# Kernel tuning notes

Hardware: AMD Instinct MI355X
Metric: run time of the kernel (lower is better)

Reference implementation:

```python
import jax, jax.numpy as jnp
import numpy as np

N = 100000
E = 1600000
IN_DIM = 1024
H_DIM = 16
DIM2 = H_DIM * 8  # 128


def _xavier(key, shape):
    fan_in, fan_out = shape[-2], shape[-1]
    lim = (6.0 / (fan_in + fan_out)) ** 0.5
    return jax.random.uniform(key, shape, jnp.float32, -lim, lim)


def setup_inputs() -> dict:
    key = jax.random.key(0)
    ks = jax.random.split(key, 10)
    x = jax.random.normal(ks[0], (N, IN_DIM), jnp.float32)
    edge_index = jax.random.randint(ks[1], (2, E), 0, N)
    perm = jax.random.permutation(ks[2], N)
    W1 = _xavier(ks[3], (IN_DIM, DIM2)); b1 = jnp.zeros((DIM2,), jnp.float32)
    W2 = _xavier(ks[4], (DIM2, DIM2)); b2 = jnp.zeros((DIM2,), jnp.float32)
    W3 = _xavier(ks[5], (DIM2, H_DIM)); b3 = jnp.zeros((H_DIM,), jnp.float32)
    Wdo = _xavier(ks[6], (1, DIM2, DIM2)); bdo = jnp.zeros((1,), jnp.float32)
    Wdh = _xavier(ks[7], (1, H_DIM, H_DIM)); bdh = jnp.zeros((1,), jnp.float32)
    return dict(x=x, W1=W1, b1=b1, W2=W2, b2=b2, W3=W3, b3=b3,
                Wdo=Wdo, bdo=bdo, Wdh=Wdh, bdh=bdh,
                edge_index=edge_index, perm=perm)


def _graph_conv(x, W, b, src, dst, norm_src, norm_dst):
    # DGL GraphConv, norm='both': D_dst^{-1/2} A D_src^{-1/2} X W + b
    h = (x * norm_src[:, None]) @ W          # mult W first (in >= out)
    agg = jax.ops.segment_sum(h[src], dst, num_segments=N)
    return agg * norm_dst[:, None] + b


def _l2norm(x):
    n = jnp.sqrt(jnp.sum(x * x, axis=1, keepdims=True))
    return x / jnp.maximum(n, 1e-12)


def _bilinear(a, c, W, b):
    # nn.Bilinear(n_h, n_h, 1): out[n,k] = a[n] @ W[k] @ c[n] + b[k]
    return jnp.einsum('nd,kde,ne->nk', a, W, c) + b


def reference(x, W1, b1, W2, b2, W3, b3, Wdo, bdo, Wdh, bdh, edge_index, perm):
    src, dst = edge_index[0], edge_index[1]
    ones = jnp.ones((E,), jnp.float32)
    deg_out = jnp.maximum(jax.ops.segment_sum(ones, src, num_segments=N), 1.0)
    deg_in = jnp.maximum(jax.ops.segment_sum(ones, dst, num_segments=N), 1.0)
    ns, nd = deg_out ** -0.5, deg_in ** -0.5

    def encode(xin):
        o = _graph_conv(xin, W1, b1, src, dst, ns, nd)
        o = _graph_conv(o, W2, b2, src, dst, ns, nd) + o
        h = _graph_conv(o, W3, b3, src, dst, ns, nd)
        emb_o = jax.nn.relu(o)
        g_o = jax.nn.sigmoid(_l2norm(emb_o))
        emb_h = jax.nn.relu(h)
        g_h = jax.nn.sigmoid(_l2norm(emb_h))
        return h, emb_o, g_o, emb_h, g_h

    h, emb_o, g_o, emb_h, g_h = encode(x)
    h_a, emb_oa, g_oa, emb_ha, g_ha = encode(x[perm])

    def disc(c, h_pl, h_mi, W, b):
        return jnp.concatenate([_bilinear(h_pl, c, W, b), _bilinear(h_mi, c, W, b)], axis=1)

    ret_o = disc(g_o, emb_o, emb_oa, Wdo, bdo)
    ret_oa = disc(g_oa, emb_oa, emb_o, Wdo, bdo)
    ret_h = disc(g_h, emb_h, emb_ha, Wdh, bdh)
    ret_ha = disc(g_ha, emb_ha, emb_h, Wdh, bdh)
    return (h, ret_o, ret_h, ret_oa, ret_ha)
```

## Files before the change

kernel.cpp:

```cpp
#include <hip/hip_runtime.h>
#include <math.h>

#define NN 100000
#define EE 1600000
#define SCB 98

typedef __attribute__((ext_vector_type(8))) short bf16x8;
typedef __attribute__((ext_vector_type(4))) short bf16x4;
typedef __attribute__((ext_vector_type(4))) float f32x4;

__device__ __forceinline__ unsigned short f2bf(float x){
  union { float f; unsigned u; } v; v.f = x;
  unsigned r = v.u + 0x7FFFu + ((v.u >> 16) & 1u);
  return (unsigned short)(r >> 16);
}
__device__ __forceinline__ float bf2f(unsigned short h){
  union { unsigned u; float f; } v; v.u = ((unsigned)h) << 16; return v.f;
}
__device__ __forceinline__ float sigm(float x){ return 1.0f/(1.0f+__expf(-x)); }

__device__ __forceinline__ void barrier_lds_only(){
  asm volatile("s_waitcnt lgkmcnt(0)" ::: "memory");
  __builtin_amdgcn_s_barrier();
  __builtin_amdgcn_sched_barrier(0);
}

__global__ __launch_bounds__(256) void k_deg_wcvt(const int* __restrict__ src, const int* __restrict__ dst,
                      int* __restrict__ dout, int* __restrict__ din,
                      const float* __restrict__ W1, const float* __restrict__ W2,
                      const float* __restrict__ Wdo, const float* __restrict__ W3,
                      unsigned short* __restrict__ W1T, unsigned short* __restrict__ W2T,
                      unsigned short* __restrict__ WdoB, unsigned short* __restrict__ W3c){
  int b = blockIdx.x;
  if (b < EE/256){
    int e = b*256 + threadIdx.x;
    atomicAdd(&dout[src[e]],1); atomicAdd(&din[dst[e]],1);
  } else {
    int i = (b - EE/256)*256 + threadIdx.x;
    if (i < 131072){
      int c = i>>13, r = i&8191, col = r>>6, k = c*64 + (r&63);
      W1T[i] = f2bf(W1[(size_t)k*128 + col]);
    } else if (i < 147456){
      int j = i-131072;
      int c = j>>13, r = j&8191, col = r>>6, k = c*64 + (r&63);
      W2T[j] = f2bf(W2[(size_t)k*128 + col]);
    } else if (i < 163840){
      int j = i-147456;
      int c = j>>13, r = j&8191, col = r>>6, k = c*64 + (r&63);
      WdoB[j] = f2bf(Wdo[(size_t)col*128 + k]);
    } else if (i < 165888){
      int j = i-163840;
      int col = j>>7, k = j&127;
      W3c[j] = f2bf(W3[(size_t)k*16 + col]);
    }
  }
}

__global__ __launch_bounds__(1024) void k_scan1(const int* __restrict__ din, int* __restrict__ chunk,
                        int* __restrict__ bsum){
  __shared__ int wsum[16];
  int t = threadIdx.x, lane = t & 63, w = t >> 6;
  int i = blockIdx.x*1024 + t;
  int v = (i < NN) ? din[i] : 0;
  int x = v;
  #pragma unroll
  for (int off=1; off<64; off<<=1){
    int y = __shfl_up(x, off);
    if (lane>=off) x += y;
  }
  if (lane==63) wsum[w] = x;
  __syncthreads();
  int pre = 0;
  #pragma unroll
  for (int j=0;j<16;j++) if (j<w) pre += wsum[j];
  int incl = x + pre;
  if (i < NN) chunk[i] = incl;
  if (t == 1023) bsum[blockIdx.x] = incl;
}

__global__ __launch_bounds__(128) void k_scan2(const int* __restrict__ bsum, int* __restrict__ bpre,
                       int* __restrict__ row_ptr){
  __shared__ int w0tot;
  int t = threadIdx.x, lane = t & 63, w = t >> 6;
  int v = (t < SCB) ? bsum[t] : 0;
  int x = v;
  #pragma unroll
  for (int off=1; off<64; off<<=1){
    int y = __shfl_up(x, off);
    if (lane>=off) x += y;
  }
  if (w==0 && lane==63) w0tot = x;
  __syncthreads();
  int incl = x + (w ? w0tot : 0);
  if (t < SCB) bpre[t] = incl - v;
  if (t == 0) row_ptr[0] = 0;
}

__global__ __launch_bounds__(256) void k_scan3(const int* __restrict__ din, const int* __restrict__ chunk,
                       const int* __restrict__ bpre, const int* __restrict__ dout,
                       const int* __restrict__ perm,
                       int* __restrict__ row_ptr, int* __restrict__ cursor,
                       float* __restrict__ ns, float* __restrict__ nd, int* __restrict__ inv){
  int i = blockIdx.x*256 + threadIdx.x;
  if (i < NN){
    int d = din[i];
    int val = chunk[i] + bpre[i>>10];
    row_ptr[i+1] = val;
    cursor[i] = val - d;
    ns[i] = rsqrtf((float)max(dout[i],1));
    nd[i] = rsqrtf((float)max(d,1));
    inv[perm[i]] = i;
  }
}

__global__ __launch_bounds__(256) void k_fill(const int* __restrict__ src, const int* __restrict__ dst,
                       int* __restrict__ cursor, int* __restrict__ col){
  int e = blockIdx.x*256+threadIdx.x;
  if (e<EE){ int pos = atomicAdd(&cursor[dst[e]],1); col[pos] = src[e]; }
}

struct ARF { float4 a, b; };
struct ARU { bf16x8 a; };
__device__ __forceinline__ void aload(ARF& r, const float* p){
  r.a = *(const float4*)p; r.b = *(const float4*)(p+4);
}
__device__ __forceinline__ void aload(ARU& r, const unsigned short* p){
  r.a = *(const bf16x8*)p;
}
template<int IM>
__device__ __forceinline__ bf16x8 aconv(const ARF& r, float rs){
  float av[8] = {r.a.x,r.a.y,r.a.z,r.a.w,r.b.x,r.b.y,r.b.z,r.b.w};
  if constexpr (IM==1){
    #pragma unroll
    for (int i=0;i<8;i++) av[i] = sigm(fmaxf(av[i],0.0f)*rs);
  }
  bf16x8 o;
  #pragma unroll
  for (int i=0;i<8;i++) o[i] = (short)f2bf(av[i]);
  return o;
}
template<int IM>
__device__ __forceinline__ bf16x8 aconv(const ARU& r, float rs){
  if constexpr (IM==0) return r.a;
  else {
    bf16x8 o;
    #pragma unroll
    for (int i=0;i<8;i++){
      float v = sigm(fmaxf(bf2f((unsigned short)r.a[i]),0.0f)*rs);
      o[i] = (short)f2bf(v);
    }
    return o;
  }
}
__device__ __forceinline__ bf16x8 araw(const ARU& r){ return r.a; }
__device__ __forceinline__ bf16x8 araw(const ARF& r){
  bf16x8 o;
  float av[8] = {r.a.x,r.a.y,r.a.z,r.a.w,r.b.x,r.b.y,r.b.z,r.b.w};
  #pragma unroll
  for (int i=0;i<8;i++) o[i] = (short)f2bf(av[i]);
  return o;
}
template<typename T> struct ARofT;
template<> struct ARofT<float>{ using type = ARF; };
template<> struct ARofT<unsigned short>{ using type = ARU; };

template<int KDIM, int IN_MODE, int OUT_MODE, typename AT>
__global__ __launch_bounds__(256,4) void k_gemmA(
    const AT* __restrict__ A, const unsigned short* __restrict__ Wc,
    unsigned short* __restrict__ out0,
    const float* __restrict__ scale, const int* __restrict__ inv,
    const float* __restrict__ rn, int nrows,
    float* __restrict__ ro, float* __restrict__ roa,
    const unsigned short* __restrict__ W3c, const float* __restrict__ ns2,
    unsigned short* __restrict__ th)
{
  constexpr int NC = KDIM/64;
  __shared__ __align__(16) unsigned short Bs[2*128*64];
  __shared__ __align__(16) unsigned short W3s[OUT_MODE==3 ? 16*128 : 16];
  int t = threadIdx.x, wave = t>>6, lane = t&63;
  int row0 = blockIdx.x*64;
  int arow = row0 + wave*16 + (lane&15);
  int kof = (lane>>4)*8;
  int arow_c = min(arow, nrows-1);
  const AT* ap = A + (size_t)arow_c*KDIM + kof;
  float rscale = 1.0f;
  if constexpr (IN_MODE==1) rscale = rn[arow_c];

  int scol = t>>3;
  int sw = ((t&7) ^ (scol&7))<<3;

  unsigned short* b0 = &Bs[0];
  unsigned short* b1 = &Bs[128*64];
  const unsigned short* bcur = b0; unsigned short* bnxt = b1;

  f32x4 acc[8] = {};
  f32x4 acc2 = {};
  typename ARofT<AT>::type A0a{},A0b{},A1a{},A1b{},A2a{},A2b{};
  bf16x8 w0{},w1{},w2{},w3{};

  {
    const unsigned short* gp = Wc + (size_t)t*8;
    bf16x8 t0 = *(const bf16x8*)(gp);
    bf16x8 t1 = *(const bf16x8*)(gp+2048);
    bf16x8 t2 = *(const bf16x8*)(gp+4096);
    bf16x8 t3 = *(const bf16x8*)(gp+6144);
    *(bf16x8*)&b0[(0*32+scol)*64 + sw] = t0;
    *(bf16x8*)&b0[(1*32+scol)*64 + sw] = t1;
    *(bf16x8*)&b0[(2*32+scol)*64 + sw] = t2;
    *(bf16x8*)&b0[(3*32+scol)*64 + sw] = t3;
  }
  if constexpr (OUT_MODE==3){
    int wc = t>>4, wsl = t&15;
    bf16x8 v = *(const bf16x8*)(W3c + wc*128 + wsl*8);
    *(bf16x8*)&W3s[wc*128 + ((wsl ^ (wc&7))<<3)] = v;
  }
  aload(A0a, ap); aload(A0b, ap+32);
  if (NC>1){
    const unsigned short* gp = Wc + 8192 + (size_t)t*8;
    w0 = *(const bf16x8*)(gp);
    w1 = *(const bf16x8*)(gp+2048);
    w2 = *(const bf16x8*)(gp+4096);
    w3 = *(const bf16x8*)(gp+6144);
    aload(A1a, ap+64); aload(A1b, ap+96);
  }
  __syncthreads();

  int slot0 = lane>>4;
  int c = lane & 15;
  #pragma unroll
  for (int cc=0; cc<NC; ++cc){
    if (cc+2 < NC){
      aload(A2a, ap + (cc+2)*64);
      aload(A2b, ap + (cc+2)*64 + 32);
    }
    {
      bf16x8 af = aconv<IN_MODE>(A0a, rscale);
      #pragma unroll
      for (int j=0;j<8;j++){
        int cj = j*16 + c;
        bf16x8 b = *(const bf16x8*)&bcur[cj*64 + ((slot0 ^ (cj&7))<<3)];
        acc[j] = __builtin_amdgcn_mfma_f32_16x16x32_bf16(af, b, acc[j], 0, 0, 0);
      }
      if constexpr (OUT_MODE==3){
        int sl = cc*8 + slot0;
        bf16x8 b = *(const bf16x8*)&W3s[c*128 + ((sl ^ (c&7))<<3)];
        acc2 = __builtin_amdgcn_mfma_f32_16x16x32_bf16(araw(A0a), b, acc2, 0, 0, 0);
      }
    }
    {
      bf16x8 af = aconv<IN_MODE>(A0b, rscale);
      #pragma unroll
      for (int j=0;j<8;j++){
        int cj = j*16 + c;
        bf16x8 b = *(const bf16x8*)&bcur[cj*64 + (((slot0+4) ^ (cj&7))<<3)];
        acc[j] = __builtin_amdgcn_mfma_f32_16x16x32_bf16(af, b, acc[j], 0, 0, 0);
      }
      if constexpr (OUT_MODE==3){
        int sl = cc*8 + 4 + slot0;
        bf16x8 b = *(const bf16x8*)&W3s[c*128 + ((sl ^ (c&7))<<3)];
        acc2 = __builtin_amdgcn_mfma_f32_16x16x32_bf16(araw(A0b), b, acc2, 0, 0, 0);
      }
    }
    if (cc+1 < NC){
      *(bf16x8*)&bnxt[(0*32+scol)*64 + sw] = w0;
      *(bf16x8*)&bnxt[(1*32+scol)*64 + sw] = w1;
      *(bf16x8*)&bnxt[(2*32+scol)*64 + sw] = w2;
      *(bf16x8*)&bnxt[(3*32+scol)*64 + sw] = w3;
      barrier_lds_only();
      const unsigned short* tmp = bcur; bcur = bnxt; bnxt = (unsigned short*)tmp;
      if (cc+2 < NC){
        const unsigned short* gp = Wc + (size_t)(cc+2)*8192 + (size_t)t*8;
        w0 = *(const bf16x8*)(gp);
        w1 = *(const bf16x8*)(gp+2048);
        w2 = *(const bf16x8*)(gp+4096);
        w3 = *(const bf16x8*)(gp+6144);
      }
    }
    A0a=A1a; A0b=A1b; A1a=A2a; A1b=A2b;
  }

  if constexpr (OUT_MODE==3){
    #pragma unroll
    for (int r=0;r<4;r++){
      int row = row0 + wave*16 + (lane>>4)*4 + r;
      int sidx = row>=NN ? row-NN : row;
      float v = acc2[r]*ns2[sidx];
      size_t tof = row<NN ? (size_t)row*32 + c : (size_t)(row-NN)*32 + 16 + c;
      th[tof] = f2bf(v);
    }
    __syncthreads();
    unsigned short* Os = &Bs[0];
    unsigned short* Oo = &Bs[8192];
    for (int p=t; p<2048; p+=256){
      int r = (p>>4)&63, seg = p&15;
      int row = row0 + r;
      int srcrow = (p<1024) ? row : (row<NN ? row+NN : row-NN);
      unsigned short* dst = (p<1024) ? Os : Oo;
      *(bf16x8*)&dst[r*128 + ((seg ^ (r&7))<<3)] = *(const bf16x8*)&A[(size_t)srcrow*128 + seg*8];
    }
    __syncthreads();
    float bb = scale[0];
    #pragma unroll
    for (int r=0;r<4;r++){
      int lr = wave*16 + (lane>>4)*4 + r;
      float dsame=0.f, doth=0.f;
      #pragma unroll
      for (int j=0;j<8;j++){
        float v = acc[j][r];
        int colj = j*16 + c;
        int idx = lr*128 + (((colj>>3) ^ (lr&7))<<3) + (colj&7);
        dsame += fmaxf(bf2f(Os[idx]),0.f)*v;
        doth  += fmaxf(bf2f(Oo[idx]),0.f)*v;
      }
      #pragma unroll
      for (int off=1; off<16; off<<=1){
        dsame += __shfl_xor(dsame, off);
        doth  += __shfl_xor(doth, off);
      }
      if (c==0){
        int row = row0 + lr;
        if (row < NN){
          ro[(size_t)row*2+0] = dsame + bb;
          ro[(size_t)row*2+1] = doth + bb;
        } else {
          int m = row - NN;
          roa[(size_t)m*2+0] = dsame + bb;
          roa[(size_t)m*2+1] = doth + bb;
        }
      }
    }
  } else {
    int rbase = row0 + wave*16 + (lane>>4)*4;
    #pragma unroll
    for (int j=0;j<8;j++){
      int colx = j*16 + c;
      #pragma unroll
      for (int r=0;r<4;r++){
        int row = rbase + r;
        if (row < nrows){
          float v = acc[j][r];
          if constexpr (OUT_MODE==0){
            out0[(size_t)row*256 + colx] = f2bf(v * scale[row]);
            int ir = inv[row];
            out0[(size_t)ir*256 + 128 + colx] = f2bf(v * scale[ir]);
          } else {
            int sidx = row >= NN ? row - NN : row;
            size_t zof = row < NN ? (size_t)row*256 + colx : (size_t)(row-NN)*256 + 128 + colx;
            out0[zof] = f2bf(v * scale[sidx]);
          }
        }
      }
    }
  }
}

template<bool RESID>
__global__ __launch_bounds__(256) void k_agg128(
  const unsigned short* __restrict__ z,
  const int* __restrict__ row_ptr, const int* __restrict__ col,
  const float* __restrict__ nd, const float* __restrict__ bias,
  unsigned short* __restrict__ ob, float* __restrict__ rn)
{
  int wave = threadIdx.x>>6, lane = threadIdx.x&63;
  int row = blockIdx.x*4 + wave;
  if (row >= NN) return;
  int s = row_ptr[row], e = row_ptr[row+1];
  int es = lane>>5;
  int half = (lane>>4)&1;
  int c8 = (lane&15)*8;
  size_t lof = (size_t)half*128 + c8;
  float acc[8] = {};
  int i = s + es;
  int sc0 = (i < e) ? col[i] : -1;
  int sc1 = (i+2 < e) ? col[i+2] : -1;
  bf16x8 u0 = {}, u1 = {};
  if (sc0 >= 0) u0 = *(const bf16x8*)(z + (size_t)sc0*256 + lof);
  if (sc1 >= 0) u1 = *(const bf16x8*)(z + (size_t)sc1*256 + lof);
  while (sc0 >= 0){
    int ni = i + 4;
    int nsc0 = (ni < e) ? col[ni] : -1;
    int nsc1 = (ni+2 < e) ? col[ni+2] : -1;
    bf16x8 v0 = {}, v1 = {};
    if (nsc0 >= 0) v0 = *(const bf16x8*)(z + (size_t)nsc0*256 + lof);
    if (nsc1 >= 0) v1 = *(const bf16x8*)(z + (size_t)nsc1*256 + lof);
    #pragma unroll
    for (int j=0;j<8;j++) acc[j] += bf2f((unsigned short)u0[j]);
    if (sc1 >= 0){
      #pragma unroll
      for (int j=0;j<8;j++) acc[j] += bf2f((unsigned short)u1[j]);
    }
    u0 = v0; u1 = v1; sc0 = nsc0; sc1 = nsc1; i = ni;
  }
  #pragma unroll
  for (int j=0;j<8;j++) acc[j] += __shfl_down(acc[j], 32);
  if (lane < 32){
    float ndr = nd[row];
    size_t oof = half ? (size_t)(NN+row)*128 + c8 : (size_t)row*128 + c8;
    float ra[8];
    #pragma unroll
    for (int j=0;j<8;j++) ra[j] = acc[j]*ndr + bias[c8+j];
    if constexpr (RESID){
      bf16x8 pv = *(const bf16x8*)(ob + oof);
      #pragma unroll
      for (int j=0;j<8;j++) ra[j] += bf2f((unsigned short)pv[j]);
    }
    bf16x8 wv;
    #pragma unroll
    for (int j=0;j<8;j++) wv[j] = (short)f2bf(ra[j]);
    *(bf16x8*)(ob + oof) = wv;
    if constexpr (RESID){
      float sa = 0.f;
      #pragma unroll
      for (int j=0;j<8;j++){ float x1 = fmaxf(ra[j],0.f); sa += x1*x1; }
      sa += __shfl_down(sa, 8);
      sa += __shfl_down(sa, 4);
      sa += __shfl_down(sa, 2);
      sa += __shfl_down(sa, 1);
      if ((lane&15)==0) rn[half ? NN+row : row] = 1.0f/fmaxf(sqrtf(sa),1e-12f);
    }
  }
}

__global__ __launch_bounds__(256) void k_agg16(
  const unsigned short* __restrict__ th,
  const int* __restrict__ row_ptr, const int* __restrict__ col,
  const float* __restrict__ nd, const float* __restrict__ b3,
  float* __restrict__ hout, float* __restrict__ h2)
{
  int wave = threadIdx.x>>6, lane = threadIdx.x&63;
  int row = blockIdx.x*4 + wave;
  if (row >= NN) return;
  int s = row_ptr[row], e = row_ptr[row+1];
  int es = lane>>3, l8 = lane&7;
  float a4[4] = {};
  int i = s + es;
  int sc0 = (i<e)? col[i] : -1;
  int sc1 = (i+8<e)? col[i+8] : -1;
  bf16x4 u0 = {}, u1 = {};
  if (sc0 >= 0) u0 = *(const bf16x4*)(th + (size_t)sc0*32 + l8*4);
  if (sc1 >= 0) u1 = *(const bf16x4*)(th + (size_t)sc1*32 + l8*4);
  while (sc0 >= 0){
    int ni = i + 16;
    int nsc0 = (ni<e)? col[ni] : -1;
    int nsc1 = (ni+8<e)? col[ni+8] : -1;
    bf16x4 v0 = {}, v1 = {};
    if (nsc0 >= 0) v0 = *(const bf16x4*)(th + (size_t)nsc0*32 + l8*4);
    if (nsc1 >= 0) v1 = *(const bf16x4*)(th + (size_t)nsc1*32 + l8*4);
    #pragma unroll
    for (int j=0;j<4;j++) a4[j] += bf2f((unsigned short)u0[j]);
    if (sc1 >= 0){
      #pragma unroll
      for (int j=0;j<4;j++) a4[j] += bf2f((unsigned short)u1[j]);
    }
    u0 = v0; u1 = v1; sc0 = nsc0; sc1 = nsc1; i = ni;
  }
  #pragma unroll
  for (int j=0;j<4;j++){
    a4[j] += __shfl_down(a4[j], 32);
    a4[j] += __shfl_down(a4[j], 16);
    a4[j] += __shfl_down(a4[j], 8);
  }
  if (lane < 8){
    float ndr = nd[row];
    int half = l8>>2, c0 = (l8&3)*4;
    float4 r;
    r.x = a4[0]*ndr + b3[c0+0];
    r.y = a4[1]*ndr + b3[c0+1];
    r.z = a4[2]*ndr + b3[c0+2];
    r.w = a4[3]*ndr + b3[c0+3];
    if (half==0) *(float4*)&hout[(size_t)row*16 + c0] = r;
    else         *(float4*)&h2  [(size_t)row*16 + c0] = r;
  }
}

__global__ __launch_bounds__(256) void k_ret_h(const float* __restrict__ h1, const float* __restrict__ h2,
  const float* __restrict__ Wdh, const float* __restrict__ bdh,
  float* __restrict__ rh, float* __restrict__ rha)
{
  __shared__ float Ws[256];
  int t = threadIdx.x;
  if (t<256) Ws[t]=Wdh[t];
  __syncthreads();
  int n = blockIdx.x*256 + t;
  if (n>=NN) return;
  float e1[16], e2[16];
  float s1=0.f, s2=0.f;
  const float* p1 = h1 + (size_t)n*16;
  const float* p2 = h2 + (size_t)n*16;
  #pragma unroll
  for (int i=0;i<16;i++){
    e1[i]=fmaxf(p1[i],0.f); s1+=e1[i]*e1[i];
    e2[i]=fmaxf(p2[i],0.f); s2+=e2[i]*e2[i];
  }
  float r1 = 1.0f/fmaxf(sqrtf(s1),1e-12f);
  float r2 = 1.0f/fmaxf(sqrtf(s2),1e-12f);
  float g1[16], g2[16];
  #pragma unroll
  for (int i=0;i<16;i++){ g1[i]=sigm(e1[i]*r1); g2[i]=sigm(e2[i]*r2); }
  float q00=0.f,q01=0.f,q10=0.f,q11=0.f;
  #pragma unroll
  for (int d=0; d<16; d++){
    float vh1=0.f, vh2=0.f;
    #pragma unroll
    for (int e=0;e<16;e++){ vh1 += Ws[d*16+e]*g1[e]; vh2 += Ws[d*16+e]*g2[e]; }
    q00 += e1[d]*vh1; q01 += e2[d]*vh1;
    q10 += e2[d]*vh2; q11 += e1[d]*vh2;
  }
  float bb = bdh[0];
  rh [(size_t)n*2+0]=q00+bb; rh [(size_t)n*2+1]=q01+bb;
  rha[(size_t)n*2+0]=q10+bb; rha[(size_t)n*2+1]=q11+bb;
}

extern "C" void kernel_launch(void* const* d_in, const int* in_sizes, int n_in,
                              void* d_out, int out_size, void* d_ws, size_t ws_size,
                              hipStream_t stream){
  const float* x   = (const float*)d_in[0];
  const float* W1  = (const float*)d_in[1];
  const float* b1  = (const float*)d_in[2];
  const float* W2  = (const float*)d_in[3];
  const float* b2  = (const float*)d_in[4];
  const float* W3  = (const float*)d_in[5];
  const float* b3  = (const float*)d_in[6];
  const float* Wdo = (const float*)d_in[7];
  const float* bdo = (const float*)d_in[8];
  const float* Wdh = (const float*)d_in[9];
  const float* bdh = (const float*)d_in[10];
  const int* ei    = (const int*)d_in[11];
  const int* perm  = (const int*)d_in[12];
  const int* esrc = ei;
  const int* edst = ei + EE;

  char* ws = (char*)d_ws;
  size_t off = 0;
  auto alloc = [&](size_t bytes)->void*{ void* p = ws + off; off += (bytes + 255) & ~(size_t)255; return p; };
  unsigned short* z  = (unsigned short*)alloc((size_t)NN*256*2);
  unsigned short* ob = (unsigned short*)alloc((size_t)2*NN*128*2);
  unsigned short* th = (unsigned short*)alloc((size_t)NN*32*2);
  float* h2 = (float*)alloc((size_t)NN*16*4);
  int* deg = (int*)alloc((size_t)2*NN*4);
  int* dout_ = deg; int* din_ = deg + NN;
  float* ns = (float*)alloc((size_t)NN*4);
  float* nd = (float*)alloc((size_t)NN*4);
  int* inv  = (int*)alloc((size_t)NN*4);
  float* rn = (float*)alloc((size_t)2*NN*4);
  int* cursor = (int*)alloc((size_t)NN*4);
  int* row_ptr = (int*)alloc((size_t)(NN+1)*4);
  int* colx = (int*)alloc((size_t)EE*4);
  int* chunk = (int*)alloc((size_t)NN*4);
  int* bsum = (int*)alloc((size_t)SCB*4);
  int* bpre = (int*)alloc((size_t)SCB*4);
  unsigned short* W1T = (unsigned short*)alloc((size_t)1024*128*2);
  unsigned short* W2T = (unsigned short*)alloc((size_t)128*128*2);
  unsigned short* WdoB = (unsigned short*)alloc((size_t)128*128*2);
  unsigned short* W3c = (unsigned short*)alloc((size_t)16*128*2);

  float* out_h   = (float*)d_out;
  float* out_ro  = out_h  + (size_t)NN*16;
  float* out_rh  = out_ro + (size_t)NN*2;
  float* out_roa = out_rh + (size_t)NN*2;
  float* out_rha = out_roa+ (size_t)NN*2;

  hipMemsetAsync(deg, 0, (size_t)2*NN*4, stream);
  k_deg_wcvt<<<EE/256 + 648, 256, 0, stream>>>(esrc, edst, dout_, din_,
                                               W1, W2, Wdo, W3, W1T, W2T, WdoB, W3c);
  k_scan1<<<SCB, 1024, 0, stream>>>(din_, chunk, bsum);
  k_scan2<<<1, 128, 0, stream>>>(bsum, bpre, row_ptr);
  k_scan3<<<(NN+255)/256, 256, 0, stream>>>(din_, chunk, bpre, dout_, perm, row_ptr, cursor, ns, nd, inv);
  k_fill<<<EE/256, 256, 0, stream>>>(esrc, edst, cursor, colx);

  int gb1 = (NN + 63)/64;
  int gb2 = (2*NN)/64;
  k_gemmA<1024,0,0,float><<<gb1,256,0,stream>>>(x, W1T, z, ns, inv, nullptr, NN,
                                                nullptr, nullptr, nullptr, nullptr, nullptr);
  k_agg128<false><<<(NN+3)/4,256,0,stream>>>(z, row_ptr, colx, nd, b1, ob, nullptr);
  k_gemmA<128,0,1,unsigned short><<<gb2,256,0,stream>>>(ob, W2T, z, ns, nullptr, nullptr, 2*NN,
                                                nullptr, nullptr, nullptr, nullptr, nullptr);
  k_agg128<true><<<(NN+3)/4,256,0,stream>>>(z, row_ptr, colx, nd, b2, ob, rn);
  k_gemmA<128,1,3,unsigned short><<<gb2,256,0,stream>>>(ob, WdoB, nullptr, bdo, nullptr, rn, 2*NN,
                                                out_ro, out_roa, W3c, ns, th);
  k_agg16<<<(NN+3)/4,256,0,stream>>>(th, row_ptr, colx, nd, b3, out_h, h2);
  k_ret_h<<<(NN+255)/256,256,0,stream>>>(out_h, h2, Wdh, bdh, out_rh, out_rha);
}
```

Before: 749.2 us.

## Use direct global-to-LDS weight loads, deepen gather prefetch, fuse ret_h into agg16

The GEMM kernel now streams weight tiles straight into LDS with global_load_lds and vmcnt waits. This replaces staging them through registers plus ds_write, and the weight pre-conversion kernel pre-swizzles the layout to match. The 128-wide aggregation kernel prefetches two edge pairs ahead instead of one to hide gather latency. The final bilinear discriminator for h is fused into the 16-wide aggregation kernel via LDS and shuffles, which removes a launch and the h2 round trip, at the cost of LDS traffic and partial-wave work.

```diff
diff --git a/kernel.cpp b/kernel.cpp
--- a/kernel.cpp
+++ b/kernel.cpp
@@ -19,11 +19,19 @@
 }
 __device__ __forceinline__ float sigm(float x){ return 1.0f/(1.0f+__expf(-x)); }
 
-__device__ __forceinline__ void barrier_lds_only(){
-  asm volatile("s_waitcnt lgkmcnt(0)" ::: "memory");
-  __builtin_amdgcn_s_barrier();
-  __builtin_amdgcn_sched_barrier(0);
-}
+__device__ __forceinline__ void gload16(const unsigned short* g, unsigned short* l){
+  __builtin_amdgcn_global_load_lds(
+    (const __attribute__((address_space(1))) void*)g,
+    (__attribute__((address_space(3))) void*)l, 16, 0, 0);
+}
+template<int N>
+__device__ __forceinline__ void waitvm(){
+  if constexpr (N==0) asm volatile("s_waitcnt vmcnt(0)" ::: "memory");
+  else if constexpr (N==2) asm volatile("s_waitcnt vmcnt(2)" ::: "memory");
+  else if constexpr (N==4) asm volatile("s_waitcnt vmcnt(4)" ::: "memory");
+  else if constexpr (N==8) asm volatile("s_waitcnt vmcnt(8)" ::: "memory");
+}
+__device__ __forceinline__ void membar(){ asm volatile("" ::: "memory"); }
 
 __global__ __launch_bounds__(256) void k_deg_wcvt(const int* __restrict__ src, const int* __restrict__ dst,
                       int* __restrict__ dout, int* __restrict__ din,
@@ -38,15 +46,21 @@
   } else {
     int i = (b - EE/256)*256 + threadIdx.x;
     if (i < 131072){
-      int c = i>>13, r = i&8191, col = r>>6, k = c*64 + (r&63);
+      int c = i>>13, s = i&8191;
+      int col = s>>6, p = (s>>3)&7, e2 = s&7;
+      int k = c*64 + 8*(p ^ (col&7)) + e2;
       W1T[i] = f2bf(W1[(size_t)k*128 + col]);
     } else if (i < 147456){
       int j = i-131072;
-      int c = j>>13, r = j&8191, col = r>>6, k = c*64 + (r&63);
+      int c = j>>13, s = j&8191;
+      int col = s>>6, p = (s>>3)&7, e2 = s&7;
+      int k = c*64 + 8*(p ^ (col&7)) + e2;
       W2T[j] = f2bf(W2[(size_t)k*128 + col]);
     } else if (i < 163840){
       int j = i-147456;
-      int c = j>>13, r = j&8191, col = r>>6, k = c*64 + (r&63);
+      int c = j>>13, s = j&8191;
+      int col = s>>6, p = (s>>3)&7, e2 = s&7;
+      int k = c*64 + 8*(p ^ (col&7)) + e2;
       WdoB[j] = f2bf(Wdo[(size_t)col*128 + k]);
     } else if (i < 165888){
       int j = i-163840;
@@ -175,8 +189,10 @@
     unsigned short* __restrict__ th)
 {
   constexpr int NC = KDIM/64;
-  __shared__ __align__(16) unsigned short Bs[2*128*64];
-  __shared__ __align__(16) unsigned short W3s[OUT_MODE==3 ? 16*128 : 16];
+  constexpr int APC = (sizeof(AT)==4) ? 4 : 2;
+  constexpr int BSSZ = 2*128*64 + (OUT_MODE==3 ? 2048 : 0);
+  __shared__ __align__(16) unsigned short Bs[BSSZ];
+  unsigned short* W3s = &Bs[16384];
   int t = threadIdx.x, wave = t>>6, lane = t&63;
   int row0 = blockIdx.x*64;
   int arow = row0 + wave*16 + (lane&15);
@@ -186,9 +202,6 @@
   float rscale = 1.0f;
   if constexpr (IN_MODE==1) rscale = rn[arow_c];
 
-  int scol = t>>3;
-  int sw = ((t&7) ^ (scol&7))<<3;
-
   unsigned short* b0 = &Bs[0];
   unsigned short* b1 = &Bs[128*64];
   const unsigned short* bcur = b0; unsigned short* bnxt = b1;
@@ -196,43 +209,43 @@
   f32x4 acc[8] = {};
   f32x4 acc2 = {};
   typename ARofT<AT>::type A0a{},A0b{},A1a{},A1b{},A2a{},A2b{};
-  bf16x8 w0{},w1{},w2{},w3{};
-
-  {
-    const unsigned short* gp = Wc + (size_t)t*8;
-    bf16x8 t0 = *(const bf16x8*)(gp);
-    bf16x8 t1 = *(const bf16x8*)(gp+2048);
-    bf16x8 t2 = *(const bf16x8*)(gp+4096);
-    bf16x8 t3 = *(const bf16x8*)(gp+6144);
-    *(bf16x8*)&b0[(0*32+scol)*64 + sw] = t0;
-    *(bf16x8*)&b0[(1*32+scol)*64 + sw] = t1;
-    *(bf16x8*)&b0[(2*32+scol)*64 + sw] = t2;
-    *(bf16x8*)&b0[(3*32+scol)*64 + sw] = t3;
-  }
+
   if constexpr (OUT_MODE==3){
     int wc = t>>4, wsl = t&15;
     bf16x8 v = *(const bf16x8*)(W3c + wc*128 + wsl*8);
     *(bf16x8*)&W3s[wc*128 + ((wsl ^ (wc&7))<<3)] = v;
   }
+  membar();
+  {
+    unsigned short* lb = b0 + wave*2048;
+    const unsigned short* gb = Wc + wave*2048 + lane*8;
+    #pragma unroll
+    for (int q=0;q<4;q++) gload16(gb + q*512, lb + q*512);
+  }
+  membar();
   aload(A0a, ap); aload(A0b, ap+32);
-  if (NC>1){
-    const unsigned short* gp = Wc + 8192 + (size_t)t*8;
-    w0 = *(const bf16x8*)(gp);
-    w1 = *(const bf16x8*)(gp+2048);
-    w2 = *(const bf16x8*)(gp+4096);
-    w3 = *(const bf16x8*)(gp+6144);
-    aload(A1a, ap+64); aload(A1b, ap+96);
-  }
-  __syncthreads();
+  if (NC>1){ aload(A1a, ap+64); aload(A1b, ap+96); }
+  waitvm<2*APC>();
+  asm volatile("s_waitcnt lgkmcnt(0)" ::: "memory");
+  __builtin_amdgcn_s_barrier();
+  __builtin_amdgcn_sched_barrier(0);
 
   int slot0 = lane>>4;
   int c = lane & 15;
   #pragma unroll
   for (int cc=0; cc<NC; ++cc){
+    if (cc+1 < NC){
+      unsigned short* lb = bnxt + wave*2048;
+      const unsigned short* gb = Wc + (size_t)(cc+1)*8192 + wave*2048 + lane*8;
+      #pragma unroll
+      for (int q=0;q<4;q++) gload16(gb + q*512, lb + q*512);
+    }
+    membar();
     if (cc+2 < NC){
       aload(A2a, ap + (cc+2)*64);
       aload(A2b, ap + (cc+2)*64 + 32);
     }
+    membar();
     {
       bf16x8 af = aconv<IN_MODE>(A0a, rscale);
       #pragma unroll
@@ -262,19 +275,10 @@
       }
     }
     if (cc+1 < NC){
-      *(bf16x8*)&bnxt[(0*32+scol)*64 + sw] = w0;
-      *(bf16x8*)&bnxt[(1*32+scol)*64 + sw] = w1;
-      *(bf16x8*)&bnxt[(2*32+scol)*64 + sw] = w2;
-      *(bf16x8*)&bnxt[(3*32+scol)*64 + sw] = w3;
-      barrier_lds_only();
+      if (cc+2 < NC) waitvm<APC>(); else waitvm<0>();
+      __builtin_amdgcn_s_barrier();
+      __builtin_amdgcn_sched_barrier(0);
       const unsigned short* tmp = bcur; bcur = bnxt; bnxt = (unsigned short*)tmp;
-      if (cc+2 < NC){
-        const unsigned short* gp = Wc + (size_t)(cc+2)*8192 + (size_t)t*8;
-        w0 = *(const bf16x8*)(gp);
-        w1 = *(const bf16x8*)(gp+2048);
-        w2 = *(const bf16x8*)(gp+4096);
-        w3 = *(const bf16x8*)(gp+6144);
-      }
     }
     A0a=A1a; A0b=A1b; A1a=A2a; A1b=A2b;
   }
@@ -371,25 +375,31 @@
   size_t lof = (size_t)half*128 + c8;
   float acc[8] = {};
   int i = s + es;
-  int sc0 = (i < e) ? col[i] : -1;
-  int sc1 = (i+2 < e) ? col[i+2] : -1;
+  int c0 = (i < e) ? col[i] : -1;
+  int c1 = (i+2 < e) ? col[i+2] : -1;
   bf16x8 u0 = {}, u1 = {};
-  if (sc0 >= 0) u0 = *(const bf16x8*)(z + (size_t)sc0*256 + lof);
-  if (sc1 >= 0) u1 = *(const bf16x8*)(z + (size_t)sc1*256 + lof);
-  while (sc0 >= 0){
-    int ni = i + 4;
-    int nsc0 = (ni < e) ? col[ni] : -1;
-    int nsc1 = (ni+2 < e) ? col[ni+2] : -1;
-    bf16x8 v0 = {}, v1 = {};
-    if (nsc0 >= 0) v0 = *(const bf16x8*)(z + (size_t)nsc0*256 + lof);
-    if (nsc1 >= 0) v1 = *(const bf16x8*)(z + (size_t)nsc1*256 + lof);
+  if (c0 >= 0) u0 = *(const bf16x8*)(z + (size_t)c0*256 + lof);
+  if (c1 >= 0) u1 = *(const bf16x8*)(z + (size_t)c1*256 + lof);
+  int d0 = (i+4 < e) ? col[i+4] : -1;
+  int d1 = (i+6 < e) ? col[i+6] : -1;
+  bf16x8 v0 = {}, v1 = {};
+  if (d0 >= 0) v0 = *(const bf16x8*)(z + (size_t)d0*256 + lof);
+  if (d1 >= 0) v1 = *(const bf16x8*)(z + (size_t)d1*256 + lof);
+  while (c0 >= 0){
+    int n0 = (i+8 < e) ? col[i+8] : -1;
+    int n1 = (i+10 < e) ? col[i+10] : -1;
+    bf16x8 w0 = {}, w1 = {};
+    if (n0 >= 0) w0 = *(const bf16x8*)(z + (size_t)n0*256 + lof);
+    if (n1 >= 0) w1 = *(const bf16x8*)(z + (size_t)n1*256 + lof);
     #pragma unroll
     for (int j=0;j<8;j++) acc[j] += bf2f((unsigned short)u0[j]);
-    if (sc1 >= 0){
+    if (c1 >= 0){
       #pragma unroll
       for (int j=0;j<8;j++) acc[j] += bf2f((unsigned short)u1[j]);
     }
-    u0 = v0; u1 = v1; sc0 = nsc0; sc1 = nsc1; i = ni;
+    c0=d0; c1=d1; u0=v0; u1=v1;
+    d0=n0; d1=n1; v0=w0; v1=w1;
+    i += 4;
   }
   #pragma unroll
   for (int j=0;j<8;j++) acc[j] += __shfl_down(acc[j], 32);
@@ -425,9 +435,16 @@
   const unsigned short* __restrict__ th,
   const int* __restrict__ row_ptr, const int* __restrict__ col,
   const float* __restrict__ nd, const float* __restrict__ b3,
-  float* __restrict__ hout, float* __restrict__ h2)
+  const float* __restrict__ Wdh, const float* __restrict__ bdh,
+  float* __restrict__ hout, float* __restrict__ rh, float* __restrict__ rha)
 {
-  int wave = threadIdx.x>>6, lane = threadIdx.x&63;
+  __shared__ float Ws[256];
+  __shared__ float hbuf[4][32];
+  __shared__ float gbuf[4][32];
+  int t = threadIdx.x;
+  Ws[t] = Wdh[t];
+  __syncthreads();
+  int wave = t>>6, lane = t&63;
   int row = blockIdx.x*4 + wave;
   if (row >= NN) return;
   int s = row_ptr[row], e = row_ptr[row+1];
@@ -469,46 +486,44 @@
     r.z = a4[2]*ndr + b3[c0+2];
     r.w = a4[3]*ndr + b3[c0+3];
     if (half==0) *(float4*)&hout[(size_t)row*16 + c0] = r;
-    else         *(float4*)&h2  [(size_t)row*16 + c0] = r;
-  }
-}
-
-__global__ __launch_bounds__(256) void k_ret_h(const float* __restrict__ h1, const float* __restrict__ h2,
-  const float* __restrict__ Wdh, const float* __restrict__ bdh,
-  float* __restrict__ rh, float* __restrict__ rha)
-{
-  __shared__ float Ws[256];
-  int t = threadIdx.x;
-  if (t<256) Ws[t]=Wdh[t];
-  __syncthreads();
-  int n = blockIdx.x*256 + t;
-  if (n>=NN) return;
-  float e1[16], e2[16];
-  float s1=0.f, s2=0.f;
-  const float* p1 = h1 + (size_t)n*16;
-  const float* p2 = h2 + (size_t)n*16;
-  #pragma unroll
-  for (int i=0;i<16;i++){
-    e1[i]=fmaxf(p1[i],0.f); s1+=e1[i]*e1[i];
-    e2[i]=fmaxf(p2[i],0.f); s2+=e2[i]*e2[i];
-  }
-  float r1 = 1.0f/fmaxf(sqrtf(s1),1e-12f);
-  float r2 = 1.0f/fmaxf(sqrtf(s2),1e-12f);
-  float g1[16], g2[16];
-  #pragma unroll
-  for (int i=0;i<16;i++){ g1[i]=sigm(e1[i]*r1); g2[i]=sigm(e2[i]*r2); }
-  float q00=0.f,q01=0.f,q10=0.f,q11=0.f;
-  #pragma unroll
-  for (int d=0; d<16; d++){
+    int hb = half*16 + c0;
+    hbuf[wave][hb+0]=r.x; hbuf[wave][hb+1]=r.y; hbuf[wave][hb+2]=r.z; hbuf[wave][hb+3]=r.w;
+  }
+  if (lane < 16){
+    int d = lane;
+    float e1v = fmaxf(hbuf[wave][d],    0.f);
+    float e2v = fmaxf(hbuf[wave][16+d], 0.f);
+    float s1 = e1v*e1v, s2 = e2v*e2v;
+    #pragma unroll
+    for (int off=1; off<16; off<<=1){
+      s1 += __shfl_xor(s1, off);
+      s2 += __shfl_xor(s2, off);
+    }
+    float r1 = 1.0f/fmaxf(sqrtf(s1),1e-12f);
+    float r2 = 1.0f/fmaxf(sqrtf(s2),1e-12f);
+    gbuf[wave][d]    = sigm(e1v*r1);
+    gbuf[wave][16+d] = sigm(e2v*r2);
     float vh1=0.f, vh2=0.f;
     #pragma unroll
-    for (int e=0;e<16;e++){ vh1 += Ws[d*16+e]*g1[e]; vh2 += Ws[d*16+e]*g2[e]; }
-    q00 += e1[d]*vh1; q01 += e2[d]*vh1;
-    q10 += e2[d]*vh2; q11 += e1[d]*vh2;
-  }
-  float bb = bdh[0];
-  rh [(size_t)n*2+0]=q00+bb; rh [(size_t)n*2+1]=q01+bb;
-  rha[(size_t)n*2+0]=q10+bb; rha[(size_t)n*2+1]=q11+bb;
+    for (int e2i=0;e2i<16;e2i++){
+      float w = Ws[d*16+e2i];
+      vh1 += w*gbuf[wave][e2i];
+      vh2 += w*gbuf[wave][16+e2i];
+    }
+    float q00 = e1v*vh1, q01 = e2v*vh1, q10 = e2v*vh2, q11 = e1v*vh2;
+    #pragma unroll
+    for (int off=1; off<16; off<<=1){
+      q00 += __shfl_xor(q00, off);
+      q01 += __shfl_xor(q01, off);
+      q10 += __shfl_xor(q10, off);
+      q11 += __shfl_xor(q11, off);
+    }
+    if (lane==0){
+      float bb = bdh[0];
+      rh [(size_t)row*2+0]=q00+bb; rh [(size_t)row*2+1]=q01+bb;
+      rha[(size_t)row*2+0]=q10+bb; rha[(size_t)row*2+1]=q11+bb;
+    }
+  }
 }
 
 extern "C" void kernel_launch(void* const* d_in, const int* in_sizes, int n_in,
@@ -536,7 +551,6 @@
   unsigned short* z  = (unsigned short*)alloc((size_t)NN*256*2);
   unsigned short* ob = (unsigned short*)alloc((size_t)2*NN*128*2);
   unsigned short* th = (unsigned short*)alloc((size_t)NN*32*2);
-  float* h2 = (float*)alloc((size_t)NN*16*4);
   int* deg = (int*)alloc((size_t)2*NN*4);
   int* dout_ = deg; int* din_ = deg + NN;
   float* ns = (float*)alloc((size_t)NN*4);
@@ -578,6 +592,5 @@
   k_agg128<true><<<(NN+3)/4,256,0,stream>>>(z, row_ptr, colx, nd, b2, ob, rn);
   k_gemmA<128,1,3,unsigned short><<<gb2,256,0,stream>>>(ob, WdoB, nullptr, bdo, nullptr, rn, 2*NN,
                                                 out_ro, out_roa, W3c, ns, th);
-  k_agg16<<<(NN+3)/4,256,0,stream>>>(th, row_ptr, colx, nd, b3, out_h, h2);
-  k_ret_h<<<(NN+255)/256,256,0,stream>>>(out_h, h2, Wdh, bdh, out_rh, out_rha);
-}
+  k_agg16<<<(NN+3)/4,256,0,stream>>>(th, row_ptr, colx, nd, b3, Wdh, bdh, out_h, out_rh, out_rha);
+}
```

Result: no change. 761.2 us (+1.6%).
